# Kernel optimization log

Measured on AMD Instinct MI355X. Metric: run time of the kernel, lower is better.

Reference implementation:

```python
import jax, jax.numpy as jnp
import numpy as np

DEPTH = 7  # leaves = 2**(DEPTH-1) = 64

def setup_inputs() -> dict:
    key = jax.random.key(0)
    k1, k2, k3 = jax.random.split(key, 3)
    bs, dimx, dimy = 32768, 2048, 2048
    leaves = 2 ** (DEPTH - 1)
    x = jax.random.normal(k1, (bs, dimx), dtype=jnp.float32)
    w = 0.1 * jax.random.uniform(k2, (dimx, leaves - 1), dtype=jnp.float32)
    b = jnp.zeros((leaves - 1,), dtype=jnp.float32)
    responses = 0.1 * jax.random.uniform(k3, (leaves, dimy), dtype=jnp.float32)
    return {"x": x, "w": w, "b": b, "responses": responses}

def reference(x, w, b, responses):
    bs = x.shape[0]
    # gate probabilities for all internal nodes of the binary tree: [bs, leaves-1]
    gate = jax.nn.sigmoid(x @ w + b)
    running = jnp.ones((bs, 1), dtype=x.dtype)
    for i in range(1, DEPTH):
        parents = gate[:, 2 ** (i - 1) - 1: 2 ** i - 1]  # [bs, 2**(i-1)]
        # torch.stack([left, right], dim=1).reshape -> [left | right] concat order
        running = jnp.concatenate([parents * running, (1.0 - parents) * running], axis=1)
    return running @ responses  # [bs, dimy]
```

## Files before the change

### kernel.cpp

```cpp
#include <hip/hip_runtime.h>
#include <hip/hip_bf16.h>


typedef short bf16x8 __attribute__((ext_vector_type(8)));
typedef float f32x4  __attribute__((ext_vector_type(4)));

#define BS    32768
#define DIMX  2048
#define NODES 63
#define NL    64
#define DIMY  2048

__device__ __forceinline__ unsigned short f2bf(float f) {
    union { float f; unsigned int u; } v; v.f = f;
    unsigned int r = v.u + 0x7FFFu + ((v.u >> 16) & 1u);
    return (unsigned short)(r >> 16);
}
__device__ __forceinline__ float bf2f(unsigned short h) {
    union { float f; unsigned int u; } v; v.u = ((unsigned int)h) << 16;
    return v.f;
}

__global__ __launch_bounds__(256) void rt_conv(const float* __restrict__ R,
                                               unsigned short* __restrict__ RT) {
    int f = blockIdx.x * 256 + threadIdx.x;
    int n = f >> 6;
    int k = f & 63;
    RT[f] = f2bf(R[k * DIMY + n]);
}

__global__ __launch_bounds__(256) void wt_conv(const float* __restrict__ w,
                                               unsigned short* __restrict__ wTh,
                                               unsigned short* __restrict__ wTl) {
    int f = blockIdx.x * 256 + threadIdx.x;
    int n = f >> 11;
    int k = f & 2047;
    float v = (n < NODES) ? w[(size_t)k * NODES + n] : 0.0f;
    unsigned short h = f2bf(v);
    wTh[f] = h;
    wTl[f] = f2bf(v - bf2f(h));
}

#define GBM   32
#define GBK   64
#define GLD   72
#define NSTEP (DIMX / GBK)

__device__ __forceinline__ bf16x8 pack8(float4 a, float4 b) {
    union { __hip_bfloat162 h2[4]; bf16x8 v; } u;
    u.h2[0] = __float22bfloat162_rn(make_float2(a.x, a.y));
    u.h2[1] = __float22bfloat162_rn(make_float2(a.z, a.w));
    u.h2[2] = __float22bfloat162_rn(make_float2(b.x, b.y));
    u.h2[3] = __float22bfloat162_rn(make_float2(b.z, b.w));
    return u.v;
}

__global__ __launch_bounds__(256, 5) void gate_kernel(const float* __restrict__ x,
                                                      const unsigned short* __restrict__ wTh,
                                                      const unsigned short* __restrict__ wTl,
                                                      const float* __restrict__ bias,
                                                      unsigned short* __restrict__ P) {
    __shared__ __align__(16) unsigned short xs[GBM][GLD];
    __shared__ __align__(16) unsigned short wsh[NL][GLD];
    __shared__ __align__(16) unsigned short wsl[NL][GLD];
    __shared__ float gl[GBM][NL + 1];

    const int t    = threadIdx.x;
    const int lane = t & 63;
    const int wv   = t >> 6;
    const int lr   = lane & 15;
    const int lg   = lane >> 4;
    const int m0   = blockIdx.x * GBM;
    const int rm   = wv & 1;
    const int cfp  = wv >> 1;

    const int xr = t >> 3;
    const int xc = (t & 7) * 8;
    const float* xsrc = x + (size_t)(m0 + xr) * DIMX + xc;
    const int wrA = t >> 3;
    const int wrB = wrA + 32;
    const int wc  = (t & 7) * 8;
    const unsigned short* hA = wTh + (size_t)wrA * DIMX + wc;
    const unsigned short* hB = wTh + (size_t)wrB * DIMX + wc;
    const unsigned short* lA = wTl + (size_t)wrA * DIMX + wc;
    const unsigned short* lB = wTl + (size_t)wrB * DIMX + wc;

    float4 rx0 = *(const float4*)(xsrc);
    float4 rx1 = *(const float4*)(xsrc + 4);
    uint4  rhA = *(const uint4*)(hA);
    uint4  rhB = *(const uint4*)(hB);
    uint4  rlA = *(const uint4*)(lA);
    uint4  rlB = *(const uint4*)(lB);

    f32x4 acc[2];
    acc[0] = (f32x4){0.f, 0.f, 0.f, 0.f};
    acc[1] = (f32x4){0.f, 0.f, 0.f, 0.f};

    for (int k = 0; k < NSTEP; ++k) {
        __syncthreads();
        *(bf16x8*)&xs[xr][xc]  = pack8(rx0, rx1);
        *(uint4*)&wsh[wrA][wc] = rhA;
        *(uint4*)&wsh[wrB][wc] = rhB;
        *(uint4*)&wsl[wrA][wc] = rlA;
        *(uint4*)&wsl[wrB][wc] = rlB;
        __syncthreads();
        if (k + 1 < NSTEP) {
            const int ko = (k + 1) * GBK;
            rx0 = *(const float4*)(xsrc + ko);
            rx1 = *(const float4*)(xsrc + ko + 4);
            rhA = *(const uint4*)(hA + ko);
            rhB = *(const uint4*)(hB + ko);
            rlA = *(const uint4*)(lA + ko);
            rlB = *(const uint4*)(lB + ko);
        }
        #pragma unroll
        for (int kk = 0; kk < GBK; kk += 32) {
            bf16x8 a = *(const bf16x8*)&xs[rm * 16 + lr][kk + lg * 8];
            #pragma unroll
            for (int ci = 0; ci < 2; ++ci) {
                const int brow = (cfp * 2 + ci) * 16 + lr;
                bf16x8 bh = *(const bf16x8*)&wsh[brow][kk + lg * 8];
                bf16x8 bo = *(const bf16x8*)&wsl[brow][kk + lg * 8];
                acc[ci] = __builtin_amdgcn_mfma_f32_16x16x32_bf16(a, bh, acc[ci], 0, 0, 0);
                acc[ci] = __builtin_amdgcn_mfma_f32_16x16x32_bf16(a, bo, acc[ci], 0, 0, 0);
            }
        }
    }

    #pragma unroll
    for (int ci = 0; ci < 2; ++ci) {
        const int col = cfp * 32 + ci * 16 + lr;
        const float bb = bias[col < NODES ? col : 0];
        #pragma unroll
        for (int i = 0; i < 4; ++i) {
            int row = rm * 16 + lg * 4 + i;
            float s = acc[ci][i] + bb;
            gl[row][col] = 1.0f / (1.0f + __expf(-s));
        }
    }
    __syncthreads();

    {
        const int rr  = t >> 3;
        const int sub = t & 7;
        const int b5 = sub & 1, b4 = (sub >> 1) & 1, mh = sub >> 2;
        const float* g = gl[rr];
        float a2[2], a4[4], a8[8];
        float g0 = g[0];
        a2[0] = g0; a2[1] = 1.f - g0;
        #pragma unroll
        for (int m = 0; m < 4; ++m) {
            float gg = g[1 + (m & 1)];
            a4[m] = a2[m & 1] * ((m & 2) ? (1.f - gg) : gg);
        }
        #pragma unroll
        for (int m = 0; m < 8; ++m) {
            float gg = g[3 + (m & 3)];
            a8[m] = a4[m & 3] * ((m & 4) ? (1.f - gg) : gg);
        }
        unsigned short o[8];
        #pragma unroll
        for (int j = 0; j < 8; ++j) {
            int m = mh * 8 + j;
            float g4 = g[7 + j];
            float p  = a8[j] * (mh ? (1.f - g4) : g4);
            float g5 = g[15 + m];
            p *= b4 ? (1.f - g5) : g5;
            float g6 = g[31 + m + 16 * b4];
            p *= b5 ? (1.f - g6) : g6;
            o[j] = f2bf(p);
        }
        uint4 q;
        q.x = (unsigned)o[0] | ((unsigned)o[1] << 16);
        q.y = (unsigned)o[2] | ((unsigned)o[3] << 16);
        q.z = (unsigned)o[4] | ((unsigned)o[5] << 16);
        q.w = (unsigned)o[6] | ((unsigned)o[7] << 16);
        *(uint4*)&P[(size_t)(m0 + rr) * NL + b5 * 32 + b4 * 16 + mh * 8] = q;
    }
}

#define OBM  128
#define OBN  128
#define OLD  72

__global__ __launch_bounds__(256) void out_kernel(const unsigned short* __restrict__ P,
                                                  const unsigned short* __restrict__ RT,
                                                  float* __restrict__ out) {
    __shared__ __align__(16) unsigned short ps[OBM][OLD];
    __shared__ __align__(16) unsigned short rs[OBN][OLD];
    const int t  = threadIdx.x;
    const int n0 = blockIdx.x * OBN;
    const int m0 = blockIdx.y * OBM;

    #pragma unroll
    for (int p = 0; p < 4; ++p) {
        int c   = p * 256 + t;
        int row = c >> 3;
        int c8  = c & 7;
        *(uint4*)&ps[row][c8 * 8] = *(const uint4*)&P [(size_t)(m0 + row) * NL + c8 * 8];
        *(uint4*)&rs[row][c8 * 8] = *(const uint4*)&RT[(size_t)(n0 + row) * NL + c8 * 8];
    }
    __syncthreads();

    const int lane = t & 63;
    const int wv   = t >> 6;
    const int wm   = (wv >> 1) * 64;
    const int wn   = (wv & 1) * 64;
    const int lr   = lane & 15;
    const int lg   = lane >> 4;

    f32x4 acc[4][4];
    #pragma unroll
    for (int rf = 0; rf < 4; ++rf)
        #pragma unroll
        for (int cf = 0; cf < 4; ++cf) acc[rf][cf] = (f32x4){0.f, 0.f, 0.f, 0.f};

    #pragma unroll
    for (int kk = 0; kk < NL; kk += 32) {
        bf16x8 a[4], bb[4];
        #pragma unroll
        for (int rf = 0; rf < 4; ++rf)
            a[rf] = *(const bf16x8*)&ps[wm + rf * 16 + lr][kk + lg * 8];
        #pragma unroll
        for (int cf = 0; cf < 4; ++cf)
            bb[cf] = *(const bf16x8*)&rs[wn + cf * 16 + lr][kk + lg * 8];
        #pragma unroll
        for (int rf = 0; rf < 4; ++rf)
            #pragma unroll
            for (int cf = 0; cf < 4; ++cf)
                acc[rf][cf] = __builtin_amdgcn_mfma_f32_16x16x32_bf16(a[rf], bb[cf],
                                                                      acc[rf][cf], 0, 0, 0);
    }

    #pragma unroll
    for (int rf = 0; rf < 4; ++rf) {
        #pragma unroll
        for (int cf = 0; cf < 4; ++cf) {
            #pragma unroll
            for (int i = 0; i < 4; ++i) {
                int row = m0 + wm + rf * 16 + lg * 4 + i;
                int col = n0 + wn + cf * 16 + lr;
                out[(size_t)row * DIMY + col] = acc[rf][cf][i];
            }
        }
    }
}

extern "C" void kernel_launch(void* const* d_in, const int* in_sizes, int n_in,
                              void* d_out, int out_size, void* d_ws, size_t ws_size,
                              hipStream_t stream) {
    const float* x = (const float*)d_in[0];
    const float* w = (const float*)d_in[1];
    const float* b = (const float*)d_in[2];
    const float* R = (const float*)d_in[3];
    float* out = (float*)d_out;

    char* ws = (char*)d_ws;
    unsigned short* P   = (unsigned short*)ws;
    unsigned short* RT  = (unsigned short*)(ws + (size_t)BS * NL * 2);
    unsigned short* wTh = (unsigned short*)(ws + (size_t)BS * NL * 2 + 262144);
    unsigned short* wTl = (unsigned short*)(ws + (size_t)BS * NL * 2 + 524288);

    rt_conv<<<dim3((NL * DIMY) / 256), 256, 0, stream>>>(R, RT);
    wt_conv<<<dim3((NL * DIMX) / 256), 256, 0, stream>>>(w, wTh, wTl);
    gate_kernel<<<dim3(BS / GBM), 256, 0, stream>>>(x, wTh, wTl, b, P);
    out_kernel<<<dim3(DIMY / OBN, BS / OBM), 256, 0, stream>>>(P, RT, out);
}
```

Measured before the change: 150.1 us.

## Fuse gate and output GEMMs into one kernel with pre-swizzled responses

Merges the gate computation and the leaf-probability times responses GEMM into a single kernel. Path probabilities now stay in LDS instead of being written to and reread from global memory. Responses are prepacked into the MFMA fragment layout so each wave loads B operands straight from global with a one-step register prefetch. The two prep kernels are merged into one launch to save launch overhead. In exchange, each block streams the whole 256KB response matrix from L2 for only 32 rows, and occupancy drops from 5 to 4 blocks.

```diff
diff --git a/kernel.cpp b/kernel.cpp
--- a/kernel.cpp
+++ b/kernel.cpp
@@ -21,24 +21,29 @@
     return v.f;
 }
 
-__global__ __launch_bounds__(256) void rt_conv(const float* __restrict__ R,
-                                               unsigned short* __restrict__ RT) {
-    int f = blockIdx.x * 256 + threadIdx.x;
-    int n = f >> 6;
-    int k = f & 63;
-    RT[f] = f2bf(R[k * DIMY + n]);
-}
-
-__global__ __launch_bounds__(256) void wt_conv(const float* __restrict__ w,
-                                               unsigned short* __restrict__ wTh,
-                                               unsigned short* __restrict__ wTl) {
-    int f = blockIdx.x * 256 + threadIdx.x;
-    int n = f >> 11;
-    int k = f & 2047;
-    float v = (n < NODES) ? w[(size_t)k * NODES + n] : 0.0f;
-    unsigned short h = f2bf(v);
-    wTh[f] = h;
-    wTl[f] = f2bf(v - bf2f(h));
+__global__ __launch_bounds__(256) void prep(const float* __restrict__ w,
+                                            const float* __restrict__ R,
+                                            unsigned short* __restrict__ wTh,
+                                            unsigned short* __restrict__ wTl,
+                                            unsigned short* __restrict__ RTs) {
+    int bid = blockIdx.x;
+    int f = (bid & 511) * 256 + threadIdx.x;
+    if (bid < 512) {
+        int n = f >> 11;
+        int k = f & 2047;
+        float v = (n < NODES) ? w[(size_t)k * NODES + n] : 0.0f;
+        unsigned short h = f2bf(v);
+        wTh[f] = h;
+        wTl[f] = f2bf(v - bf2f(h));
+    } else {
+        int e  = f & 7;
+        int l  = (f >> 3) & 63;
+        int kh = (f >> 9) & 1;
+        int nf = f >> 10;
+        int k  = kh * 32 + (l >> 4) * 8 + e;
+        int n  = nf * 16 + (l & 15);
+        RTs[f] = f2bf(R[(size_t)k * DIMY + n]);
+    }
 }
 
 #define GBM   32
@@ -55,11 +60,12 @@
     return u.v;
 }
 
-__global__ __launch_bounds__(256, 5) void gate_kernel(const float* __restrict__ x,
-                                                      const unsigned short* __restrict__ wTh,
-                                                      const unsigned short* __restrict__ wTl,
-                                                      const float* __restrict__ bias,
-                                                      unsigned short* __restrict__ P) {
+__global__ __launch_bounds__(256, 4) void fused_kernel(const float* __restrict__ x,
+                                                       const unsigned short* __restrict__ wTh,
+                                                       const unsigned short* __restrict__ wTl,
+                                                       const float* __restrict__ bias,
+                                                       const unsigned short* __restrict__ RTs,
+                                                       float* __restrict__ out) {
     __shared__ __align__(16) unsigned short xs[GBM][GLD];
     __shared__ __align__(16) unsigned short wsh[NL][GLD];
     __shared__ __align__(16) unsigned short wsl[NL][GLD];
@@ -175,75 +181,54 @@
         q.y = (unsigned)o[2] | ((unsigned)o[3] << 16);
         q.z = (unsigned)o[4] | ((unsigned)o[5] << 16);
         q.w = (unsigned)o[6] | ((unsigned)o[7] << 16);
-        *(uint4*)&P[(size_t)(m0 + rr) * NL + b5 * 32 + b4 * 16 + mh * 8] = q;
-    }
-}
-
-#define OBM  128
-#define OBN  128
-#define OLD  72
-
-__global__ __launch_bounds__(256) void out_kernel(const unsigned short* __restrict__ P,
-                                                  const unsigned short* __restrict__ RT,
-                                                  float* __restrict__ out) {
-    __shared__ __align__(16) unsigned short ps[OBM][OLD];
-    __shared__ __align__(16) unsigned short rs[OBN][OLD];
-    const int t  = threadIdx.x;
-    const int n0 = blockIdx.x * OBN;
-    const int m0 = blockIdx.y * OBM;
-
+        *(uint4*)&xs[rr][b5 * 32 + b4 * 16 + mh * 8] = q;
+    }
+    __syncthreads();
+
+    bf16x8 pa[2][2];
     #pragma unroll
-    for (int p = 0; p < 4; ++p) {
-        int c   = p * 256 + t;
-        int row = c >> 3;
-        int c8  = c & 7;
-        *(uint4*)&ps[row][c8 * 8] = *(const uint4*)&P [(size_t)(m0 + row) * NL + c8 * 8];
-        *(uint4*)&rs[row][c8 * 8] = *(const uint4*)&RT[(size_t)(n0 + row) * NL + c8 * 8];
-    }
-    __syncthreads();
-
-    const int lane = t & 63;
-    const int wv   = t >> 6;
-    const int wm   = (wv >> 1) * 64;
-    const int wn   = (wv & 1) * 64;
-    const int lr   = lane & 15;
-    const int lg   = lane >> 4;
-
-    f32x4 acc[4][4];
+    for (int rf = 0; rf < 2; ++rf)
+        #pragma unroll
+        for (int kh = 0; kh < 2; ++kh)
+            pa[rf][kh] = *(const bf16x8*)&xs[rf * 16 + lr][kh * 32 + lg * 8];
+
+    const unsigned short* bbase = RTs + (size_t)(wv * 4) * 512 + (size_t)lane * 8;
+    #define BLD(s, ci, kh) (*(const bf16x8*)(bbase + (size_t)(((s) * 16 + (ci) * 2 + (kh))) * 512))
+
+    bf16x8 cur[4], nxt[4];
+    cur[0] = BLD(0, 0, 0); cur[1] = BLD(0, 0, 1);
+    cur[2] = BLD(0, 1, 0); cur[3] = BLD(0, 1, 1);
+
+    float* op = out + (size_t)(m0 + lg * 4) * DIMY + wv * 32 + lr;
+
     #pragma unroll
-    for (int rf = 0; rf < 4; ++rf)
-        #pragma unroll
-        for (int cf = 0; cf < 4; ++cf) acc[rf][cf] = (f32x4){0.f, 0.f, 0.f, 0.f};
-
-    #pragma unroll
-    for (int kk = 0; kk < NL; kk += 32) {
-        bf16x8 a[4], bb[4];
-        #pragma unroll
-        for (int rf = 0; rf < 4; ++rf)
-            a[rf] = *(const bf16x8*)&ps[wm + rf * 16 + lr][kk + lg * 8];
-        #pragma unroll
-        for (int cf = 0; cf < 4; ++cf)
-            bb[cf] = *(const bf16x8*)&rs[wn + cf * 16 + lr][kk + lg * 8];
-        #pragma unroll
-        for (int rf = 0; rf < 4; ++rf)
+    for (int s = 0; s < 16; ++s) {
+        if (s + 1 < 16) {
+            nxt[0] = BLD(s + 1, 0, 0); nxt[1] = BLD(s + 1, 0, 1);
+            nxt[2] = BLD(s + 1, 1, 0); nxt[3] = BLD(s + 1, 1, 1);
+        }
+        f32x4 oa[2][2];
+        #pragma unroll
+        for (int rf = 0; rf < 2; ++rf)
             #pragma unroll
-            for (int cf = 0; cf < 4; ++cf)
-                acc[rf][cf] = __builtin_amdgcn_mfma_f32_16x16x32_bf16(a[rf], bb[cf],
-                                                                      acc[rf][cf], 0, 0, 0);
-    }
-
-    #pragma unroll
-    for (int rf = 0; rf < 4; ++rf) {
-        #pragma unroll
-        for (int cf = 0; cf < 4; ++cf) {
+            for (int ci = 0; ci < 2; ++ci) {
+                oa[rf][ci] = (f32x4){0.f, 0.f, 0.f, 0.f};
+                oa[rf][ci] = __builtin_amdgcn_mfma_f32_16x16x32_bf16(pa[rf][0], cur[ci * 2 + 0],
+                                                                     oa[rf][ci], 0, 0, 0);
+                oa[rf][ci] = __builtin_amdgcn_mfma_f32_16x16x32_bf16(pa[rf][1], cur[ci * 2 + 1],
+                                                                     oa[rf][ci], 0, 0, 0);
+            }
+        #pragma unroll
+        for (int rf = 0; rf < 2; ++rf)
             #pragma unroll
-            for (int i = 0; i < 4; ++i) {
-                int row = m0 + wm + rf * 16 + lg * 4 + i;
-                int col = n0 + wn + cf * 16 + lr;
-                out[(size_t)row * DIMY + col] = acc[rf][cf][i];
-            }
-        }
-    }
+            for (int ci = 0; ci < 2; ++ci)
+                #pragma unroll
+                for (int i = 0; i < 4; ++i)
+                    op[(size_t)(rf * 16 + i) * DIMY + s * 128 + ci * 16] = oa[rf][ci][i];
+        #pragma unroll
+        for (int q = 0; q < 4; ++q) cur[q] = nxt[q];
+    }
+    #undef BLD
 }
 
 extern "C" void kernel_launch(void* const* d_in, const int* in_sizes, int n_in,
@@ -256,13 +241,10 @@
     float* out = (float*)d_out;
 
     char* ws = (char*)d_ws;
-    unsigned short* P   = (unsigned short*)ws;
-    unsigned short* RT  = (unsigned short*)(ws + (size_t)BS * NL * 2);
-    unsigned short* wTh = (unsigned short*)(ws + (size_t)BS * NL * 2 + 262144);
-    unsigned short* wTl = (unsigned short*)(ws + (size_t)BS * NL * 2 + 524288);
-
-    rt_conv<<<dim3((NL * DIMY) / 256), 256, 0, stream>>>(R, RT);
-    wt_conv<<<dim3((NL * DIMX) / 256), 256, 0, stream>>>(w, wTh, wTl);
-    gate_kernel<<<dim3(BS / GBM), 256, 0, stream>>>(x, wTh, wTl, b, P);
-    out_kernel<<<dim3(DIMY / OBN, BS / OBM), 256, 0, stream>>>(P, RT, out);
-}
+    unsigned short* wTh = (unsigned short*)ws;
+    unsigned short* wTl = (unsigned short*)(ws + 262144);
+    unsigned short* RTs = (unsigned short*)(ws + 524288);
+
+    prep<<<dim3(1024), 256, 0, stream>>>(w, R, wTh, wTl, RTs);
+    fused_kernel<<<dim3(BS / GBM), 256, 0, stream>>>(x, wTh, wTl, b, RTs, out);
+}
```

After: 154.1 us. +2.6%, slower.
